# Kernel tuning notes

Hardware: AMD Instinct MI355X
Metric: run time of the kernel (lower is better)

## Reference

```python
import jax, jax.numpy as jnp
import numpy as np
from jax import lax

NUM_STEPS = 32
NUM_CLASSES = 10
HIDDEN = 1024


def setup_inputs() -> dict:
    key = jax.random.key(0)
    ks = jax.random.split(key, 4)
    B, H, W, C = 8, 1024, 2048, 4
    x = jax.random.normal(ks[0], (B, H, W, C), dtype=jnp.float32)
    conv_w = jax.random.normal(ks[1], (C,), dtype=jnp.float32) * 0.5
    conv_b = jnp.zeros((1,), dtype=jnp.float32)
    w1 = jax.random.normal(ks[2], (HIDDEN, W), dtype=jnp.float32) * (1.0 / np.sqrt(W))
    b1 = jnp.zeros((HIDDEN,), dtype=jnp.float32)
    w2 = jax.random.normal(ks[3], (NUM_CLASSES, HIDDEN), dtype=jnp.float32) * (1.0 / np.sqrt(HIDDEN))
    b2 = jnp.zeros((NUM_CLASSES,), dtype=jnp.float32)
    beta1 = jnp.full((1,), 0.95, dtype=jnp.float32)
    thr1 = jnp.ones((1,), dtype=jnp.float32)
    beta2 = jnp.full((1,), 0.95, dtype=jnp.float32)
    thr2 = jnp.ones((1,), dtype=jnp.float32)
    return {"x": x, "conv_w": conv_w, "conv_b": conv_b, "w1": w1, "b1": b1,
            "beta1": beta1, "thr1": thr1, "w2": w2, "b2": b2,
            "beta2": beta2, "thr2": thr2}


def _leaky_scan(inp_t, beta, thr):
    # inp_t: [T, ...]; snntorch Leaky, reset_mechanism='subtract', reset_delay=False
    b = jnp.clip(beta, 0.0, 1.0)

    def step(mem, u):
        mem = b * mem + u
        spk = (mem > thr).astype(u.dtype)   # heaviside spike
        mem = mem - spk * thr               # subtract reset (no delay)
        return mem, spk

    mem0 = jnp.zeros(inp_t.shape[1:], dtype=inp_t.dtype)
    _, spks = lax.scan(step, mem0, inp_t)
    return spks  # [T, ...]


def reference(x, conv_w, conv_b, w1, b1, beta1, thr1, w2, b2, beta2, thr2):
    # x: [B, H, W, 4]; 1x1 conv over 4 antenna channels -> 1 channel
    xf = jnp.einsum('bhwc,c->bhw', x, conv_w) + conv_b[0]       # [B, H, W]
    B, H, W = xf.shape
    G = H // NUM_STEPS
    xr = xf.reshape(B, G, NUM_STEPS, W)                          # [B, G, T, 2048]
    h = jnp.einsum('bgtw,dw->bgtd', xr, w1) + b1                 # [B, G, T, D]
    spks1 = _leaky_scan(jnp.moveaxis(h, 2, 0), beta1, thr1)      # [T, B, G, D]
    s = spks1.sum(axis=0)                                        # [B, G, D]
    h2 = jnp.einsum('bgd,cd->bgc', s, w2) + b2                   # [B, G, C]
    spks2 = _leaky_scan(jnp.moveaxis(h2, 1, 0), beta2, thr2)     # [G, B, C]
    logits = spks2.sum(axis=0)                                   # [B, C]
    return jax.nn.softmax(logits, axis=1)
```

## Files before the change

kernel.cpp:

```cpp
#include <hip/hip_runtime.h>

#define TSTEPS 32
#define HID 1024
#define NCLS 10
#define BATCH 8
#define GGRP 32
#define MROWS 8192
#define GK 2048
#define GN 1024
#define BUFSH 24576
#define CLDS 40

typedef __attribute__((ext_vector_type(8))) short bf16x8;
typedef __attribute__((ext_vector_type(16))) float f32x16;

__device__ __forceinline__ unsigned short bf16_rne(float v) {
    unsigned u = __builtin_bit_cast(unsigned, v);
    return (unsigned short)((u + 0x7FFFu + ((u >> 16) & 1u)) >> 16);
}
__device__ __forceinline__ float bf16_f(unsigned short h) {
    unsigned u = (unsigned)h << 16;
    return __builtin_bit_cast(float, u);
}
__device__ __forceinline__ void gload16(const unsigned short* g, unsigned short* l) {
    __builtin_amdgcn_global_load_lds(
        (const __attribute__((address_space(1))) void*)g,
        (__attribute__((address_space(3))) void*)l, 16, 0, 0);
}


__global__ __launch_bounds__(256) void conv_pack_kernel(
    const float4* __restrict__ x, const float* __restrict__ cw,
    const float* __restrict__ cb,
    unsigned short* __restrict__ Ahi, unsigned short* __restrict__ Alo)
{
    __shared__ __align__(16) unsigned short lh[128 * CLDS];
    __shared__ __align__(16) unsigned short ll[128 * CLDS];
    const int rb = blockIdx.x >> 6;
    const int kb = blockIdx.x & 63;
    const float c0 = cw[0], c1 = cw[1], c2 = cw[2], c3 = cw[3], cbv = cb[0];
    const int tid = threadIdx.x;

#pragma unroll
    for (int p = 0; p < 16; ++p) {
        int i = p * 256 + tid;
        int row = i >> 5, px = i & 31;
        float4 a = x[(size_t)(rb * 128 + row) * 2048 + kb * 32 + px];
        float v = a.x * c0 + a.y * c1 + a.z * c2 + a.w * c3 + cbv;
        unsigned short h = bf16_rne(v);
        lh[row * CLDS + px] = h;
        ll[row * CLDS + px] = bf16_rne(v - bf16_f(h));
    }
    __syncthreads();

#pragma unroll
    for (int cc = 0; cc < 2; ++cc) {
        int c = tid + cc * 256;
        int u = c >> 6, w = c & 63;
        int row = (u >> 1) * 32 + (w & 31);
        int ko  = (u & 1) * 2 + (w >> 5);
        bf16x8 h8 = *(const bf16x8*)(lh + row * CLDS + ko * 8);
        bf16x8 l8 = *(const bf16x8*)(ll + row * CLDS + ko * 8);
        size_t off = ((size_t)blockIdx.x * 512 + c) * 8;
        *(bf16x8*)(Ahi + off) = h8;
        *(bf16x8*)(Alo + off) = l8;
    }
}

__global__ __launch_bounds__(256) void wpack_kernel(
    const float* __restrict__ wsrc, unsigned short* __restrict__ Bhi,
    unsigned short* __restrict__ Blo)
{
    const int kb  = blockIdx.x & 63;
    const int cbk = blockIdx.x >> 6;
    const int tid = threadIdx.x;
#pragma unroll
    for (int cc = 0; cc < 4; ++cc) {
        int c = tid + cc * 256;
        int u = c >> 6, w = c & 63;
        int col = cbk * 256 + (u >> 1) * 32 + (w & 31);
        int k0  = kb * 32 + (u & 1) * 16 + (w >> 5) * 8;
        const float* pw = wsrc + ((size_t)col * 2048 + k0);
        bf16x8 h8, l8;
#pragma unroll
        for (int e = 0; e < 8; ++e) {
            float v = pw[e];
            unsigned short h = bf16_rne(v);
            h8[e] = (short)h;
            l8[e] = (short)bf16_rne(v - bf16_f(h));
        }
        size_t off = ((size_t)blockIdx.x * 1024 + c) * 8;
        *(bf16x8*)(Bhi + off) = h8;
        *(bf16x8*)(Blo + off) = l8;
    }
}

__global__ __launch_bounds__(512) void gemm_scan_kernel(
    const unsigned short* __restrict__ Ahi, const unsigned short* __restrict__ Alo,
    const unsigned short* __restrict__ Bhi, const unsigned short* __restrict__ Blo,
    const float* __restrict__ bias,
    const float* __restrict__ beta1, const float* __restrict__ thr1,
    float* __restrict__ S)
{
    __shared__ __align__(16) unsigned short sm[3 * BUFSH];

    const int tid = threadIdx.x;
    const int lane = tid & 63, wv = tid >> 6;
    const int wr = wv >> 2, wc = wv & 3;
    const int by = blockIdx.x & 63;
    const int bx = blockIdx.x >> 6;

    const unsigned short* gAh = Ahi + (size_t)by * 262144;
    const unsigned short* gAl = Alo + (size_t)by * 262144;
    const unsigned short* gBh = Bhi + (size_t)bx * 524288;
    const unsigned short* gBl = Blo + (size_t)bx * 524288;

    f32x16 acc[2][2];
#pragma unroll
    for (int i = 0; i < 2; ++i)
#pragma unroll
        for (int j = 0; j < 2; ++j) acc[i][j] = (f32x16)0.f;

    bf16x8 fr[2][16];

#define STAGE(buf, kb_)                                                          \
    {                                                                            \
        unsigned short* dst = sm + (buf) * BUFSH;                                \
        const size_t ao = (size_t)(kb_) * 4096 + tid * 8;                        \
        const size_t bo = (size_t)(kb_) * 8192 + tid * 8;                        \
        gload16(gAh + ao, dst + tid * 8);                                        \
        gload16(gAl + ao, dst + 4096 + tid * 8);                                 \
        gload16(gBh + bo, dst + 8192 + tid * 8);                                 \
        gload16(gBh + bo + 4096, dst + 12288 + tid * 8);                         \
        gload16(gBl + bo, dst + 16384 + tid * 8);                                \
        gload16(gBl + bo + 4096, dst + 20480 + tid * 8);                         \
    }

#define READF(s, bufp)                                                           \
    {                                                                            \
        const unsigned short* bp_ = (bufp);                                      \
        _Pragma("unroll")                                                        \
        for (int i = 0; i < 2; ++i)                                              \
            _Pragma("unroll")                                                    \
            for (int kh = 0; kh < 2; ++kh) {                                     \
                int ua = (((wr * 2 + i) * 2 + kh) << 9) + fo;                    \
                fr[s][(i * 2 + kh) * 2 + 0] = *(const bf16x8*)(bp_ + ua);        \
                fr[s][(i * 2 + kh) * 2 + 1] = *(const bf16x8*)(bp_ + 4096 + ua); \
            }                                                                    \
        _Pragma("unroll")                                                        \
        for (int j = 0; j < 2; ++j)                                              \
            _Pragma("unroll")                                                    \
            for (int kh = 0; kh < 2; ++kh) {                                     \
                int ub = (((wc * 2 + j) * 2 + kh) << 9) + fo;                    \
                fr[s][8 + (j * 2 + kh) * 2 + 0] = *(const bf16x8*)(bp_ + 8192 + ub);  \
                fr[s][8 + (j * 2 + kh) * 2 + 1] = *(const bf16x8*)(bp_ + 16384 + ub); \
            }                                                                    \
    }

#define MFMAF(s)                                                                 \
    {                                                                            \
        _Pragma("unroll")                                                        \
        for (int kh = 0; kh < 2; ++kh) {                                         \
            _Pragma("unroll")                                                    \
            for (int i = 0; i < 2; ++i)                                          \
                _Pragma("unroll")                                                \
                for (int j = 0; j < 2; ++j)                                      \
                    acc[i][j] = __builtin_amdgcn_mfma_f32_32x32x16_bf16(         \
                        fr[s][(i * 2 + kh) * 2], fr[s][8 + (j * 2 + kh) * 2],    \
                        acc[i][j], 0, 0, 0);                                     \
            _Pragma("unroll")                                                    \
            for (int i = 0; i < 2; ++i)                                          \
                _Pragma("unroll")                                                \
                for (int j = 0; j < 2; ++j)                                      \
                    acc[i][j] = __builtin_amdgcn_mfma_f32_32x32x16_bf16(         \
                        fr[s][(i * 2 + kh) * 2], fr[s][8 + (j * 2 + kh) * 2 + 1],\
                        acc[i][j], 0, 0, 0);                                     \
            _Pragma("unroll")                                                    \
            for (int i = 0; i < 2; ++i)                                          \
                _Pragma("unroll")                                                \
                for (int j = 0; j < 2; ++j)                                      \
                    acc[i][j] = __builtin_amdgcn_mfma_f32_32x32x16_bf16(         \
                        fr[s][(i * 2 + kh) * 2 + 1], fr[s][8 + (j * 2 + kh) * 2],\
                        acc[i][j], 0, 0, 0);                                     \
        }                                                                        \
    }

#define KSTEP(SC, SN, KB, DOSTAGE, VMC)                                          \
    {                                                                            \
        asm volatile("s_waitcnt vmcnt(" #VMC ")" ::: "memory");                  \
        asm volatile("s_waitcnt lgkmcnt(0)" ::: "memory");                       \
        __builtin_amdgcn_sched_barrier(0);                                       \
        __builtin_amdgcn_s_barrier();                                            \
        if (DOSTAGE) STAGE(((KB) + 2) % 3, (KB) + 2);                            \
        READF(SN, sm + ((KB) % 3) * BUFSH);                                      \
        MFMAF(SC);                                                               \
        if (DOSTAGE) __builtin_amdgcn_sched_group_barrier(0x10, 6, 0);           \
        __builtin_amdgcn_sched_group_barrier(0x100, 16, 0);                      \
        __builtin_amdgcn_sched_group_barrier(0x8, 24, 0);                        \
    }

    STAGE(0, 0);
    STAGE(1, 1);
    STAGE(2, 2);
    asm volatile("s_waitcnt vmcnt(12)" ::: "memory");
    __builtin_amdgcn_s_barrier();
    const int fo = ((lane & 31) + 32 * (lane >> 5)) * 8;
    READF(0, sm);

    for (int kb = 1; kb < 61; kb += 2) {
        KSTEP(0, 1, kb, 1, 6);
        KSTEP(1, 0, kb + 1, 1, 6);
    }
    KSTEP(0, 1, 61, 1, 6);
    KSTEP(1, 0, 62, 0, 6);
    KSTEP(0, 1, 63, 0, 0);
    asm volatile("s_waitcnt lgkmcnt(0)" ::: "memory");
    __builtin_amdgcn_sched_barrier(0);
    MFMAF(1);
    __syncthreads();

    float* sb = (float*)sm;
    const float bclamp = fminf(fmaxf(beta1[0], 0.f), 1.f);
    const float th = thr1[0];
    const int sbg = tid >> 8;
    const int scol = tid & 255;
    const float bv = bias[bx * 256 + scol];

#pragma unroll
    for (int band = 0; band < 2; ++band) {
        if (wr == band) {
#pragma unroll
            for (int i = 0; i < 2; ++i)
#pragma unroll
                for (int j = 0; j < 2; ++j)
#pragma unroll
                    for (int r = 0; r < 16; ++r) {
                        int lr = i * 32 + (r & 3) + 8 * (r >> 2) + 4 * (lane >> 5);
                        int lc = wc * 64 + j * 32 + (lane & 31);
                        sb[lr * 256 + lc] = acc[i][j][r];
                    }
        }
        __syncthreads();
        float mem = 0.f, cnt = 0.f;
#pragma unroll
        for (int t = 0; t < TSTEPS; ++t) {
            float u = sb[(sbg * 32 + t) * 256 + scol] + bv;
            mem = bclamp * mem + u;
            float spk = mem > th ? 1.f : 0.f;
            mem -= spk * th;
            cnt += spk;
        }
        int bgg = by * 4 + band * 2 + sbg;
        S[(size_t)bgg * GN + bx * 256 + scol] = cnt;
        __syncthreads();
    }
}

__global__ __launch_bounds__(256) void fc2_kernel(
    const float* __restrict__ s, const float* __restrict__ w2,
    const float* __restrict__ b2, float* __restrict__ h2)
{
    int bg  = blockIdx.x;
    int tid = threadIdx.x;
    const float* sp = s + (size_t)bg * HID;
    float part[NCLS];
#pragma unroll
    for (int c = 0; c < NCLS; ++c) part[c] = 0.f;
    for (int d = tid; d < HID; d += 256) {
        float sv = sp[d];
#pragma unroll
        for (int c = 0; c < NCLS; ++c) part[c] += sv * w2[c * HID + d];
    }
#pragma unroll
    for (int c = 0; c < NCLS; ++c)
        for (int off = 32; off > 0; off >>= 1)
            part[c] += __shfl_down(part[c], off, 64);
    __shared__ float red[NCLS][4];
    int wave = tid >> 6, lanei = tid & 63;
    if (lanei == 0)
#pragma unroll
        for (int c = 0; c < NCLS; ++c) red[c][wave] = part[c];
    __syncthreads();
    if (tid < NCLS) {
        float v = red[tid][0] + red[tid][1] + red[tid][2] + red[tid][3] + b2[tid];
        h2[bg * NCLS + tid] = v;
    }
}

__global__ __launch_bounds__(128) void scan2_kernel(
    const float* __restrict__ h2, const float* __restrict__ beta2,
    const float* __restrict__ thr2, float* __restrict__ out)
{
    __shared__ float logits[BATCH][NCLS];
    int t = threadIdx.x;
    if (t < BATCH * NCLS) {
        int b = t / NCLS, c = t % NCLS;
        float bb = fminf(fmaxf(beta2[0], 0.f), 1.f);
        float th = thr2[0];
        float mem = 0.f, lg = 0.f;
        for (int g = 0; g < GGRP; ++g) {
            float u = h2[(b * GGRP + g) * NCLS + c];
            mem = bb * mem + u;
            float spk = mem > th ? 1.f : 0.f;
            mem -= spk * th;
            lg += spk;
        }
        logits[b][c] = lg;
    }
    __syncthreads();
    if (t < BATCH) {
        float mx = -1e30f;
        for (int c = 0; c < NCLS; ++c) mx = fmaxf(mx, logits[t][c]);
        float e[NCLS];
        float sum = 0.f;
        for (int c = 0; c < NCLS; ++c) { e[c] = expf(logits[t][c] - mx); sum += e[c]; }
        for (int c = 0; c < NCLS; ++c) out[t * NCLS + c] = e[c] / sum;
    }
}

extern "C" void kernel_launch(void* const* d_in, const int* in_sizes, int n_in,
                              void* d_out, int out_size, void* d_ws, size_t ws_size,
                              hipStream_t stream)
{
    const float* x     = (const float*)d_in[0];
    const float* cw    = (const float*)d_in[1];
    const float* cb    = (const float*)d_in[2];
    const float* w1    = (const float*)d_in[3];
    const float* b1    = (const float*)d_in[4];
    const float* beta1 = (const float*)d_in[5];
    const float* thr1  = (const float*)d_in[6];
    const float* w2    = (const float*)d_in[7];
    const float* b2    = (const float*)d_in[8];
    const float* beta2 = (const float*)d_in[9];
    const float* thr2  = (const float*)d_in[10];
    float* out = (float*)d_out;

    unsigned short* ahi = (unsigned short*)d_ws;
    unsigned short* alo = ahi + (size_t)MROWS * GK;
    unsigned short* bhi = alo + (size_t)MROWS * GK;
    unsigned short* blo = bhi + (size_t)GN * GK;
    float* s  = (float*)(blo + (size_t)GN * GK);
    float* h2 = s + (size_t)BATCH * GGRP * HID;

    conv_pack_kernel<<<4096, 256, 0, stream>>>((const float4*)x, cw, cb, ahi, alo);
    wpack_kernel    <<<256, 256, 0, stream>>>(w1, bhi, blo);
    gemm_scan_kernel<<<256, 512, 0, stream>>>(ahi, alo, bhi, blo, b1, beta1, thr1, s);
    fc2_kernel      <<<256, 256, 0, stream>>>(s, w2, b2, h2);
    scan2_kernel    <<<1, 128, 0, stream>>>(h2, beta2, thr2, out);
}
```

Measured before the change: 159.2 us.

## Load B fragments directly from global to registers and shrink LDS staging

The B operand (hi and lo bf16 weight fragments) is now read straight from global memory into registers instead of being staged through LDS. Only A goes through a three-deep LDS ring, which shrinks shared memory from about 144 KB to 64 KB and allows launch_bounds(512, 2) for two blocks per CU. Block indices are also remapped so neighbouring blocks on the same XCD share B column tiles, and the explicit sched_group_barrier hints are dropped. The cost is that the two wave rows in a block each fetch the same B data, raising L2 traffic. Waits for B now depend on the compiler's register-dependency waitcnts rather than the manual vmcnt values.

```diff
diff --git a/kernel.cpp b/kernel.cpp
--- a/kernel.cpp
+++ b/kernel.cpp
@@ -8,7 +8,7 @@
 #define MROWS 8192
 #define GK 2048
 #define GN 1024
-#define BUFSH 24576
+#define ABUF 8192
 #define CLDS 40
 
 typedef __attribute__((ext_vector_type(8))) short bf16x8;
@@ -95,25 +95,27 @@
     }
 }
 
-__global__ __launch_bounds__(512) void gemm_scan_kernel(
+__global__ __launch_bounds__(512, 2) void gemm_scan_kernel(
     const unsigned short* __restrict__ Ahi, const unsigned short* __restrict__ Alo,
     const unsigned short* __restrict__ Bhi, const unsigned short* __restrict__ Blo,
     const float* __restrict__ bias,
     const float* __restrict__ beta1, const float* __restrict__ thr1,
     float* __restrict__ S)
 {
-    __shared__ __align__(16) unsigned short sm[3 * BUFSH];
+    __shared__ __align__(16) unsigned short sm[32768];
 
     const int tid = threadIdx.x;
     const int lane = tid & 63, wv = tid >> 6;
     const int wr = wv >> 2, wc = wv & 3;
-    const int by = blockIdx.x & 63;
-    const int bx = blockIdx.x >> 6;
+    const int xcd = blockIdx.x & 7;
+    const int bx = xcd >> 1;
+    const int by = (blockIdx.x >> 3) * 2 + (xcd & 1);
 
     const unsigned short* gAh = Ahi + (size_t)by * 262144;
     const unsigned short* gAl = Alo + (size_t)by * 262144;
-    const unsigned short* gBh = Bhi + (size_t)bx * 524288;
-    const unsigned short* gBl = Blo + (size_t)bx * 524288;
+    const int fo = ((lane & 31) + 32 * (lane >> 5)) * 8;
+    const unsigned short* pBh = Bhi + (size_t)bx * 524288 + fo;
+    const unsigned short* pBl = Blo + (size_t)bx * 524288 + fo;
 
     f32x16 acc[2][2];
 #pragma unroll
@@ -123,37 +125,38 @@
 
     bf16x8 fr[2][16];
 
-#define STAGE(buf, kb_)                                                          \
-    {                                                                            \
-        unsigned short* dst = sm + (buf) * BUFSH;                                \
+#define STAGE_A(buf, kb_)                                                        \
+    {                                                                            \
+        unsigned short* dst = sm + (buf) * ABUF + tid * 8;                       \
         const size_t ao = (size_t)(kb_) * 4096 + tid * 8;                        \
-        const size_t bo = (size_t)(kb_) * 8192 + tid * 8;                        \
-        gload16(gAh + ao, dst + tid * 8);                                        \
-        gload16(gAl + ao, dst + 4096 + tid * 8);                                 \
-        gload16(gBh + bo, dst + 8192 + tid * 8);                                 \
-        gload16(gBh + bo + 4096, dst + 12288 + tid * 8);                         \
-        gload16(gBl + bo, dst + 16384 + tid * 8);                                \
-        gload16(gBl + bo + 4096, dst + 20480 + tid * 8);                         \
-    }
-
-#define READF(s, bufp)                                                           \
+        gload16(gAh + ao, dst);                                                  \
+        gload16(gAl + ao, dst + 4096);                                           \
+    }
+
+#define LOADB(s, kb_)                                                            \
+    {                                                                            \
+        const unsigned short* bh_ = pBh + (size_t)(kb_) * 8192;                  \
+        const unsigned short* bl_ = pBl + (size_t)(kb_) * 8192;                  \
+        _Pragma("unroll")                                                        \
+        for (int j = 0; j < 2; ++j)                                              \
+            _Pragma("unroll")                                                    \
+            for (int kh = 0; kh < 2; ++kh) {                                     \
+                int u = (wc * 2 + j) * 2 + kh;                                   \
+                fr[s][8 + (j * 2 + kh) * 2 + 0] = *(const bf16x8*)(bh_ + u * 512); \
+                fr[s][8 + (j * 2 + kh) * 2 + 1] = *(const bf16x8*)(bl_ + u * 512); \
+            }                                                                    \
+    }
+
+#define READFA(s, bufp)                                                          \
     {                                                                            \
         const unsigned short* bp_ = (bufp);                                      \
         _Pragma("unroll")                                                        \
         for (int i = 0; i < 2; ++i)                                              \
             _Pragma("unroll")                                                    \
             for (int kh = 0; kh < 2; ++kh) {                                     \
-                int ua = (((wr * 2 + i) * 2 + kh) << 9) + fo;                    \
+                int ua = ((wr * 2 + i) * 2 + kh) * 512 + fo;                     \
                 fr[s][(i * 2 + kh) * 2 + 0] = *(const bf16x8*)(bp_ + ua);        \
                 fr[s][(i * 2 + kh) * 2 + 1] = *(const bf16x8*)(bp_ + 4096 + ua); \
-            }                                                                    \
-        _Pragma("unroll")                                                        \
-        for (int j = 0; j < 2; ++j)                                              \
-            _Pragma("unroll")                                                    \
-            for (int kh = 0; kh < 2; ++kh) {                                     \
-                int ub = (((wc * 2 + j) * 2 + kh) << 9) + fo;                    \
-                fr[s][8 + (j * 2 + kh) * 2 + 0] = *(const bf16x8*)(bp_ + 8192 + ub);  \
-                fr[s][8 + (j * 2 + kh) * 2 + 1] = *(const bf16x8*)(bp_ + 16384 + ub); \
             }                                                                    \
     }
 
@@ -191,29 +194,27 @@
         asm volatile("s_waitcnt lgkmcnt(0)" ::: "memory");                       \
         __builtin_amdgcn_sched_barrier(0);                                       \
         __builtin_amdgcn_s_barrier();                                            \
-        if (DOSTAGE) STAGE(((KB) + 2) % 3, (KB) + 2);                            \
-        READF(SN, sm + ((KB) % 3) * BUFSH);                                      \
+        LOADB(SN, KB);                                                           \
+        if (DOSTAGE) STAGE_A(((KB) + 2) % 3, (KB) + 2);                          \
+        READFA(SN, sm + ((KB) % 3) * ABUF);                                      \
         MFMAF(SC);                                                               \
-        if (DOSTAGE) __builtin_amdgcn_sched_group_barrier(0x10, 6, 0);           \
-        __builtin_amdgcn_sched_group_barrier(0x100, 16, 0);                      \
-        __builtin_amdgcn_sched_group_barrier(0x8, 24, 0);                        \
-    }
-
-    STAGE(0, 0);
-    STAGE(1, 1);
-    STAGE(2, 2);
+    }
+
+    STAGE_A(0, 0);
+    STAGE_A(1, 1);
+    STAGE_A(2, 2);
+    LOADB(0, 0);
     asm volatile("s_waitcnt vmcnt(12)" ::: "memory");
     __builtin_amdgcn_s_barrier();
-    const int fo = ((lane & 31) + 32 * (lane >> 5)) * 8;
-    READF(0, sm);
+    READFA(0, sm);
 
     for (int kb = 1; kb < 61; kb += 2) {
-        KSTEP(0, 1, kb, 1, 6);
-        KSTEP(1, 0, kb + 1, 1, 6);
-    }
-    KSTEP(0, 1, 61, 1, 6);
-    KSTEP(1, 0, 62, 0, 6);
-    KSTEP(0, 1, 63, 0, 0);
+        KSTEP(0, 1, kb, 1, 10);
+        KSTEP(1, 0, kb + 1, 1, 10);
+    }
+    KSTEP(0, 1, 61, 1, 10);
+    KSTEP(1, 0, 62, 0, 10);
+    KSTEP(0, 1, 63, 0, 8);
     asm volatile("s_waitcnt lgkmcnt(0)" ::: "memory");
     __builtin_amdgcn_sched_barrier(0);
     MFMAF(1);
```

Measured after the change: 167.0 us. 4.9% more time.
